# Kernel optimization log

Hardware: AMD Instinct MI355X
Metric: run time of the kernel (lower is better)

Reference implementation:

```python
import jax, jax.numpy as jnp
import numpy as np

KH, KW = 5, 5  # kernel_size
B, C, H, W = 4, 3, 1024, 1024


def setup_inputs() -> dict:
    key = jax.random.key(0)
    x = jax.random.normal(key, (B, C, H, W), dtype=jnp.float32)
    return {"input": x}


def _median_blur(x, kh, kw):
    # zero padding identical to _compute_zero_padding: (k-1)//2 per side -> 'same' output
    ph, pw = (kh - 1) // 2, (kw - 1) // 2
    b, c, h, w = x.shape
    xp = jnp.pad(x, ((0, 0), (0, 0), (ph, ph), (pw, pw)))
    # Materialize the kh*kw shifted views (same math as conv2d with binary kernel / im2col)
    patches = jnp.stack(
        [xp[:, :, i:i + h, j:j + w] for i in range(kh) for j in range(kw)],
        axis=2,
    )  # [B, C, kh*kw, H, W]
    # torch.median(dim=2)[0]: for odd kh*kw this is the exact middle order statistic
    sorted_p = jnp.sort(patches, axis=2)
    mid = (kh * kw - 1) // 2
    return sorted_p[:, :, mid, :, :]


def reference(input) -> jnp.ndarray:
    return _median_blur(input, KH, KW)
```

## Files before the change

### kernel.cpp

```cpp
#include <hip/hip_runtime.h>

#define CAS(a, b) { float _t = fminf(a, b); (b) = fmaxf(a, b); (a) = _t; }

__device__ __forceinline__ void sort5(float& a0, float& a1, float& a2, float& a3, float& a4) {
    CAS(a0, a1); CAS(a3, a4); CAS(a2, a4); CAS(a2, a3);
    CAS(a0, a3); CAS(a0, a2); CAS(a1, a4); CAS(a1, a3); CAS(a1, a2);
}

#define TILE_W 32
#define TILE_H 8
#define HALO   2
#define LDS_W  (TILE_W + 2 * HALO)
#define LDS_H  (TILE_H + 2 * HALO)
#define IMG_W  1024
#define IMG_H  1024

__global__ __launch_bounds__(256, 4)
void median5x5_kernel(const float* __restrict__ in, float* __restrict__ out) {
    __shared__ float tile[LDS_H][LDS_W];
    __shared__ float scol[5][TILE_H][LDS_W];

    const int tx  = threadIdx.x;
    const int ty  = threadIdx.y;
    const int tid = ty * TILE_W + tx;
    const int x0  = blockIdx.x * TILE_W;
    const int y0  = blockIdx.y * TILE_H;
    const float* plane = in + (size_t)blockIdx.z * (IMG_W * IMG_H);

    #pragma unroll
    for (int idx = tid; idx < LDS_H * LDS_W; idx += 256) {
        int r  = idx / LDS_W;
        int c  = idx - r * LDS_W;
        int gy = y0 - HALO + r;
        int gx = x0 - HALO + c;
        float v = 0.0f;
        if ((unsigned)gx < (unsigned)IMG_W && (unsigned)gy < (unsigned)IMG_H)
            v = plane[gy * IMG_W + gx];
        tile[r][c] = v;
    }
    __syncthreads();

    #pragma unroll
    for (int c = tx; c < LDS_W; c += TILE_W) {
        float c0 = tile[ty + 0][c];
        float c1 = tile[ty + 1][c];
        float c2 = tile[ty + 2][c];
        float c3 = tile[ty + 3][c];
        float c4 = tile[ty + 4][c];
        sort5(c0, c1, c2, c3, c4);
        scol[0][ty][c] = c0;
        scol[1][ty][c] = c1;
        scol[2][ty][c] = c2;
        scol[3][ty][c] = c3;
        scol[4][ty][c] = c4;
    }
    __syncthreads();

    float w[5][5];
    #pragma unroll
    for (int i = 0; i < 5; ++i)
        #pragma unroll
        for (int j = 0; j < 5; ++j)
            w[i][j] = scol[i][ty][tx + j];

    #pragma unroll
    for (int i = 0; i < 5; ++i)
        sort5(w[i][0], w[i][1], w[i][2], w[i][3], w[i][4]);


    float p = w[0][3], q = w[0][4];
    float r_ = w[1][2], s = w[1][3], t = w[1][4];
    CAS(p, r_); CAS(q, r_); CAS(r_, s);

    float x = w[3][0], y = w[3][1], z = w[3][2];
    float m = w[4][0], n = w[4][1];
    CAS(z, n); CAS(z, m); CAS(y, z);

    CAS(p, n); CAS(q, m); CAS(r_, z); CAS(s, y); CAS(t, x);

    float M01 = fmaxf(p, q),  m01 = fminf(p, q);
    float M23 = fmaxf(r_, s), m23 = fminf(r_, s);
    float max4 = fmaxf(M01, M23);
    float sec4 = fmaxf(fminf(M01, M23), fmaxf(m01, m23));
    float l2 = fmaxf(max4, t);
    float l1 = fmaxf(fminf(max4, t), sec4);

    float mn01 = fminf(n, m),  Mx01 = fmaxf(n, m);
    float mn23 = fminf(z, y),  Mx23 = fmaxf(z, y);
    float min4  = fminf(mn01, mn23);
    float sec4b = fminf(fmaxf(mn01, mn23), fminf(Mx01, Mx23));
    float u1 = fminf(min4, x);
    float u2 = fminf(fmaxf(min4, x), sec4b);

    float h0 = w[2][1], h1 = w[2][2], h2 = w[2][3];
    float E2 = fmaxf(fmaxf(l1, h0), fminf(u1, h2));
    float O1 = __builtin_amdgcn_fmed3f(l2, u2, h1);
    float med = fminf(E2, O1);

    out[(size_t)blockIdx.z * (IMG_W * IMG_H) + (size_t)(y0 + ty) * IMG_W + (x0 + tx)] = med;
}

extern "C" void kernel_launch(void* const* d_in, const int* in_sizes, int n_in,
                              void* d_out, int out_size, void* d_ws, size_t ws_size,
                              hipStream_t stream) {
    const float* in  = (const float*)d_in[0];
    float*       out = (float*)d_out;
    dim3 block(TILE_W, TILE_H, 1);
    dim3 grid(IMG_W / TILE_W, IMG_H / TILE_H, 12);
    hipLaunchKernelGGL(median5x5_kernel, grid, block, 0, stream, in, out);
}
```

Baseline: 160.4 us.

## Compute two horizontally adjacent medians per thread sharing a sorted 4-column core

Each thread now produces two adjacent output pixels. It sorts the four shared middle columns of each row once, then merges the left or right extra element into that sorted core for each pixel, so the row-sort work is shared between the two outputs. The tile widens to 64 columns: global loads become float4 and LDS reads and output stores become float2. This cuts the comparator count and instruction overhead per pixel, at the cost of twice as many live registers per thread and half as many blocks.

```diff
diff --git a/kernel.cpp b/kernel.cpp
--- a/kernel.cpp
+++ b/kernel.cpp
@@ -1,103 +1,128 @@
 #include <hip/hip_runtime.h>
 
 #define CAS(a, b) { float _t = fminf(a, b); (b) = fmaxf(a, b); (a) = _t; }
+
+#define IMG    1024
+#define TW     64
+#define TH     8
+#define RAW_W  72
+#define RAW_H  12
 
 __device__ __forceinline__ void sort5(float& a0, float& a1, float& a2, float& a3, float& a4) {
     CAS(a0, a1); CAS(a3, a4); CAS(a2, a4); CAS(a2, a3);
     CAS(a0, a3); CAS(a0, a2); CAS(a1, a4); CAS(a1, a3); CAS(a1, a2);
 }
 
-#define TILE_W 32
-#define TILE_H 8
-#define HALO   2
-#define LDS_W  (TILE_W + 2 * HALO)
-#define LDS_H  (TILE_H + 2 * HALO)
-#define IMG_W  1024
-#define IMG_H  1024
-
-__global__ __launch_bounds__(256, 4)
-void median5x5_kernel(const float* __restrict__ in, float* __restrict__ out) {
-    __shared__ float tile[LDS_H][LDS_W];
-    __shared__ float scol[5][TILE_H][LDS_W];
-
-    const int tx  = threadIdx.x;
-    const int ty  = threadIdx.y;
-    const int tid = ty * TILE_W + tx;
-    const int x0  = blockIdx.x * TILE_W;
-    const int y0  = blockIdx.y * TILE_H;
-    const float* plane = in + (size_t)blockIdx.z * (IMG_W * IMG_H);
-
-    #pragma unroll
-    for (int idx = tid; idx < LDS_H * LDS_W; idx += 256) {
-        int r  = idx / LDS_W;
-        int c  = idx - r * LDS_W;
-        int gy = y0 - HALO + r;
-        int gx = x0 - HALO + c;
-        float v = 0.0f;
-        if ((unsigned)gx < (unsigned)IMG_W && (unsigned)gy < (unsigned)IMG_H)
-            v = plane[gy * IMG_W + gx];
-        tile[r][c] = v;
-    }
-    __syncthreads();
-
-    #pragma unroll
-    for (int c = tx; c < LDS_W; c += TILE_W) {
-        float c0 = tile[ty + 0][c];
-        float c1 = tile[ty + 1][c];
-        float c2 = tile[ty + 2][c];
-        float c3 = tile[ty + 3][c];
-        float c4 = tile[ty + 4][c];
-        sort5(c0, c1, c2, c3, c4);
-        scol[0][ty][c] = c0;
-        scol[1][ty][c] = c1;
-        scol[2][ty][c] = c2;
-        scol[3][ty][c] = c3;
-        scol[4][ty][c] = c4;
-    }
-    __syncthreads();
-
-    float w[5][5];
-    #pragma unroll
-    for (int i = 0; i < 5; ++i)
-        #pragma unroll
-        for (int j = 0; j < 5; ++j)
-            w[i][j] = scol[i][ty][tx + j];
-
-    #pragma unroll
-    for (int i = 0; i < 5; ++i)
-        sort5(w[i][0], w[i][1], w[i][2], w[i][3], w[i][4]);
-
-
-    float p = w[0][3], q = w[0][4];
-    float r_ = w[1][2], s = w[1][3], t = w[1][4];
+__device__ __forceinline__ float tail13(float a03, float a04,
+                                        float a12, float a13, float a14,
+                                        float a21, float a22, float a23,
+                                        float a30, float a31, float a32,
+                                        float a40, float a41) {
+    float p = a03, q = a04, r_ = a12, s = a13, t = a14;
     CAS(p, r_); CAS(q, r_); CAS(r_, s);
-
-    float x = w[3][0], y = w[3][1], z = w[3][2];
-    float m = w[4][0], n = w[4][1];
+    float x = a30, y = a31, z = a32, m = a40, n = a41;
     CAS(z, n); CAS(z, m); CAS(y, z);
-
     CAS(p, n); CAS(q, m); CAS(r_, z); CAS(s, y); CAS(t, x);
-
     float M01 = fmaxf(p, q),  m01 = fminf(p, q);
     float M23 = fmaxf(r_, s), m23 = fminf(r_, s);
     float max4 = fmaxf(M01, M23);
     float sec4 = fmaxf(fminf(M01, M23), fmaxf(m01, m23));
     float l2 = fmaxf(max4, t);
     float l1 = fmaxf(fminf(max4, t), sec4);
-
     float mn01 = fminf(n, m),  Mx01 = fmaxf(n, m);
     float mn23 = fminf(z, y),  Mx23 = fmaxf(z, y);
     float min4  = fminf(mn01, mn23);
     float sec4b = fminf(fmaxf(mn01, mn23), fminf(Mx01, Mx23));
     float u1 = fminf(min4, x);
     float u2 = fminf(fmaxf(min4, x), sec4b);
+    float E2 = fmaxf(fmaxf(l1, a21), fminf(u1, a23));
+    float O1 = __builtin_amdgcn_fmed3f(l2, u2, a22);
+    return fminf(E2, O1);
+}
 
-    float h0 = w[2][1], h1 = w[2][2], h2 = w[2][3];
-    float E2 = fmaxf(fmaxf(l1, h0), fminf(u1, h2));
-    float O1 = __builtin_amdgcn_fmed3f(l2, u2, h1);
-    float med = fminf(E2, O1);
+__global__ __launch_bounds__(256, 4)
+void median5x5_kernel(const float* __restrict__ in, float* __restrict__ out) {
+    __shared__ float tile[RAW_H][RAW_W];
+    __shared__ float scol[5][TH][RAW_W];
 
-    out[(size_t)blockIdx.z * (IMG_W * IMG_H) + (size_t)(y0 + ty) * IMG_W + (x0 + tx)] = med;
+    const int tx  = threadIdx.x;
+    const int ty  = threadIdx.y;
+    const int tid = ty * 32 + tx;
+    const int x0  = blockIdx.x * TW;
+    const int y0  = blockIdx.y * TH;
+    const float* plane = in + (size_t)blockIdx.z * (IMG * IMG);
+
+    if (tid < RAW_H * (RAW_W / 4)) {
+        int r   = tid / 18;
+        int k   = tid - r * 18;
+        int gy  = y0 - 2 + r;
+        int gx0 = x0 - 4 + 4 * k;
+        float4 v = make_float4(0.f, 0.f, 0.f, 0.f);
+        if ((unsigned)gy < IMG && (unsigned)gx0 < IMG)
+            v = *(const float4*)(plane + (size_t)gy * IMG + gx0);
+        *(float4*)&tile[r][4 * k] = v;
+    }
+    __syncthreads();
+
+#define SORTCOL(c) { \
+        float c0 = tile[ty + 0][c], c1 = tile[ty + 1][c], c2 = tile[ty + 2][c], \
+              c3 = tile[ty + 3][c], c4 = tile[ty + 4][c]; \
+        sort5(c0, c1, c2, c3, c4); \
+        scol[0][ty][c] = c0; scol[1][ty][c] = c1; scol[2][ty][c] = c2; \
+        scol[3][ty][c] = c3; scol[4][ty][c] = c4; }
+    SORTCOL(tx + 2);
+    SORTCOL(tx + 34);
+    if (tx < 4) SORTCOL(tx + 66);
+#undef SORTCOL
+    __syncthreads();
+
+    const int cb = 2 * tx + 2;
+    float v0, v1, v2, v3, v4, v5, m0, m1, m2, m3, t1, t2;
+
+#define LOADROW(i) { \
+        const float* rp = &scol[i][ty][cb]; \
+        float2 ua = *(const float2*)rp; \
+        float2 ub = *(const float2*)(rp + 2); \
+        float2 uc = *(const float2*)(rp + 4); \
+        v0 = ua.x; v1 = ua.y; v2 = ub.x; v3 = ub.y; v4 = uc.x; v5 = uc.y; \
+        m0 = v1; m1 = v2; m2 = v3; m3 = v4; \
+        CAS(m0, m1); CAS(m2, m3); CAS(m0, m2); CAS(m1, m3); CAS(m1, m2); }
+
+    LOADROW(0);
+    float A03, A04, B03, B04;
+    A04 = fmaxf(m3, v0); A03 = fmaxf(fminf(m3, v0), m2);
+    B04 = fmaxf(m3, v5); B03 = fmaxf(fminf(m3, v5), m2);
+
+    LOADROW(1);
+    float A12, A13, A14, B12, B13, B14;
+    A14 = fmaxf(m3, v0); t1 = fminf(m3, v0); A13 = fmaxf(m2, t1); t2 = fminf(m2, t1); A12 = fmaxf(m1, t2);
+    B14 = fmaxf(m3, v5); t1 = fminf(m3, v5); B13 = fmaxf(m2, t1); t2 = fminf(m2, t1); B12 = fmaxf(m1, t2);
+
+    LOADROW(2);
+    float A21, A22, A23, B21, B22, B23;
+    A21 = fmaxf(m0, fminf(m1, v0));
+    A22 = __builtin_amdgcn_fmed3f(m1, m2, v0);
+    A23 = fminf(m3, fmaxf(m2, v0));
+    B21 = fmaxf(m0, fminf(m1, v5));
+    B22 = __builtin_amdgcn_fmed3f(m1, m2, v5);
+    B23 = fminf(m3, fmaxf(m2, v5));
+
+    LOADROW(3);
+    float A30, A31, A32, B30, B31, B32;
+    A30 = fminf(m0, v0); t1 = fmaxf(m0, v0); A31 = fminf(m1, t1); t2 = fmaxf(m1, t1); A32 = fminf(m2, t2);
+    B30 = fminf(m0, v5); t1 = fmaxf(m0, v5); B31 = fminf(m1, t1); t2 = fmaxf(m1, t1); B32 = fminf(m2, t2);
+
+    LOADROW(4);
+    float A40, A41, B40, B41;
+    A40 = fminf(m0, v0); A41 = fminf(fmaxf(m0, v0), m1);
+    B40 = fminf(m0, v5); B41 = fminf(fmaxf(m0, v5), m1);
+#undef LOADROW
+
+    float medA = tail13(A03, A04, A12, A13, A14, A21, A22, A23, A30, A31, A32, A40, A41);
+    float medB = tail13(B03, B04, B12, B13, B14, B21, B22, B23, B30, B31, B32, B40, B41);
+
+    float2 o; o.x = medA; o.y = medB;
+    *(float2*)(out + (size_t)blockIdx.z * (IMG * IMG) + (size_t)(y0 + ty) * IMG + x0 + 2 * tx) = o;
 }
 
 extern "C" void kernel_launch(void* const* d_in, const int* in_sizes, int n_in,
@@ -105,7 +130,7 @@
                               hipStream_t stream) {
     const float* in  = (const float*)d_in[0];
     float*       out = (float*)d_out;
-    dim3 block(TILE_W, TILE_H, 1);
-    dim3 grid(IMG_W / TILE_W, IMG_H / TILE_H, 12);
+    dim3 block(32, TH, 1);
+    dim3 grid(IMG / TW, IMG / TH, 12);
     hipLaunchKernelGGL(median5x5_kernel, grid, block, 0, stream, in, out);
 }
```

Result: faster. 133.3 us (-16.9%).
